# Optimization experiments

Hardware: AMD Instinct MI355X
Metric: run time of the kernel (lower is better)

## Reference

```python
import jax, jax.numpy as jnp
import numpy as np

KH = KW = 3
STRIDE = 1
PAD = 1
DIL = 1


def setup_inputs() -> dict:
    key = jax.random.key(0)
    k1, k2, k3, k4 = jax.random.split(key, 4)
    B, C, H, W = 16, 64, 64, 64
    Cout = 64
    K = KH * KW
    x = jax.random.normal(k1, (B, C, H, W), jnp.float32)
    offset = jax.random.normal(k2, (B, 2 * K, H, W), jnp.float32)
    mask = jax.random.uniform(k3, (B, K, H, W), jnp.float32)
    # uniform(-stdv, stdv) init with stdv = 1/sqrt(C*KH*KW) ~ 0.0417; scaled normal is close enough
    weight = jax.random.normal(k4, (Cout, C, KH, KW), jnp.float32) * 0.04
    bias = jnp.zeros((Cout,), jnp.float32)  # no_bias=True -> frozen zeros, still added
    return dict(input=x, offset=offset, mask=mask, weight=weight, bias=bias)


def _bilinear(img, py, px):
    # img: [C, H, W]; py, px: [K, Ho, Wo] float sampling coords
    # DCNv2 semantics: out-of-bounds corner contributions are zero.
    H, W = img.shape[1], img.shape[2]
    y0f = jnp.floor(py)
    x0f = jnp.floor(px)
    wy = py - y0f
    wx = px - x0f
    y0 = y0f.astype(jnp.int32)
    x0 = x0f.astype(jnp.int32)
    out = jnp.zeros((img.shape[0],) + py.shape, img.dtype)
    for dy in (0, 1):
        for dx in (0, 1):
            yi = y0 + dy
            xi = x0 + dx
            valid = ((yi >= 0) & (yi < H) & (xi >= 0) & (xi < W)).astype(img.dtype)
            v = img[:, jnp.clip(yi, 0, H - 1), jnp.clip(xi, 0, W - 1)]  # [C,K,Ho,Wo]
            w = (wy if dy else 1.0 - wy) * (wx if dx else 1.0 - wx)
            out = out + v * (w * valid)[None]
    return out  # [C, K, Ho, Wo]


def reference(input, offset, mask, weight, bias):
    B, C, H, W = input.shape
    Cout, _, kh, kw = weight.shape
    K = kh * kw
    Ho = (H + 2 * PAD - (DIL * (kh - 1) + 1)) // STRIDE + 1
    Wo = (W + 2 * PAD - (DIL * (kw - 1) + 1)) // STRIDE + 1
    off = offset.reshape(B, K, 2, Ho, Wo)  # per kernel point: (dy, dx)
    ky = jnp.repeat(jnp.arange(kh), kw)  # [K] kernel row index
    kx = jnp.tile(jnp.arange(kw), kh)    # [K] kernel col index
    base_y = jnp.arange(Ho) * STRIDE - PAD
    base_x = jnp.arange(Wo) * STRIDE - PAD
    py = off[:, :, 0] + (base_y[None, None, :, None] + (ky * DIL)[None, :, None, None])
    px = off[:, :, 1] + (base_x[None, None, None, :] + (kx * DIL)[None, :, None, None])
    sampled = jax.vmap(_bilinear)(input, py, px)        # [B, C, K, Ho, Wo]
    modulated = sampled * mask[:, None]                 # mask-modulated accumulation
    out = jnp.einsum('bckpq,ock->bopq', modulated, weight.reshape(Cout, C, K))
    return out + bias[None, :, None, None]
```

## Files before the change

### kernel.cpp

```cpp
#include <hip/hip_runtime.h>
#include <hip/hip_fp16.h>

#define BATCH 16
#define C_IN  64
#define HH    64
#define WW    64
#define COUT  64
#define KK    9
#define HW    4096
#define CK    576
#define MROW  200

typedef _Float16 f16x8 __attribute__((ext_vector_type(8)));
typedef float    f32x4 __attribute__((ext_vector_type(4)));

__device__ __forceinline__ unsigned short f32_to_f16u(float f) {
    _Float16 h = (_Float16)f;
    unsigned short u;
    __builtin_memcpy(&u, &h, 2);
    return u;
}

__device__ __forceinline__ __half2 as_h2(unsigned int u) {
    __half2 r; __builtin_memcpy(&r, &u, 4); return r;
}
__device__ __forceinline__ unsigned int as_u32(__half2 v) {
    unsigned int u; __builtin_memcpy(&u, &v, 4); return u;
}

__global__ __launch_bounds__(256) void prep_kernel(
    const float* __restrict__ x, const float* __restrict__ w,
    unsigned short* __restrict__ xt, unsigned short* __restrict__ wt) {
    __shared__ unsigned short tile[64][72];
    const int t = threadIdx.x;
    const int blk = blockIdx.x;
    if (blk < 1024) {
        const int b = blk >> 6, y = blk & 63;
        const float* xrow = x + ((b * 64) * 64 + y) * 64;
#pragma unroll
        for (int it = 0; it < 4; ++it) {
            const int idx = it * 256 + t;
            const int c = idx >> 4, seg = idx & 15;
            const float4 v = *(const float4*)(xrow + c * HW + seg * 4);
            tile[seg * 4 + 0][c] = f32_to_f16u(v.x);
            tile[seg * 4 + 1][c] = f32_to_f16u(v.y);
            tile[seg * 4 + 2][c] = f32_to_f16u(v.z);
            tile[seg * 4 + 3][c] = f32_to_f16u(v.w);
        }
        __syncthreads();
#pragma unroll
        for (int it = 0; it < 2; ++it) {
            const int idx = it * 256 + t;
            const int xx = idx >> 3, cs = idx & 7;
            *(int4*)&xt[((b * HW) + y * 64 + xx) * 64 + cs * 8] =
                *(const int4*)&tile[xx][cs * 8];
        }
    } else {
        const int i = (blk - 1024) * 256 + t;
        const int j = i & 7;
        const int l = (i >> 3) & 63;
        const int ot = (i >> 9) & 3;
        const int r = i >> 11;
        const int ks = r % 6, kc = r / 6;
        const int o  = ot * 16 + (l & 15);
        const int kk = ks * 32 + (l >> 4) * 8 + j;
        const int tap = kk >> 6, c = kk & 63;
        const int k = kc * 3 + tap;
        wt[i] = f32_to_f16u(w[o * CK + c * KK + k]);
    }
}

__global__ __launch_bounds__(128, 4) void dcn_main_kernel(
    const float* __restrict__ offset, const float* __restrict__ mask,
    const unsigned short* __restrict__ xt, const unsigned short* __restrict__ wt,
    const float* __restrict__ bias, float* __restrict__ out) {
    __shared__ __align__(16) unsigned short Mlds[2][16 * MROW];
    __shared__ __align__(16) int PWw[2][144 * 4];
    __shared__ __align__(8) unsigned short PWa[2][144 * 4];

    const int t    = threadIdx.x;
    const int wave = __builtin_amdgcn_readfirstlane(t >> 6);
    const int lane = t & 63;
    const int quad = lane >> 4, m16 = lane & 15;

    const int blk = blockIdx.x;
    const int xcd = blk & 7;
    const int i8  = blk >> 3;
    const int s   = ((i8 & 31) << 3) | (i8 >> 5);
    const int b   = (xcd << 1) | (s >> 7);
    const int rr  = s & 127;
    const int row = rr >> 1;
    const int qbase = (rr & 1) * 32 + wave * 16;

    f32x4 acc[4];
#pragma unroll
    for (int ot = 0; ot < 4; ++ot)
#pragma unroll
        for (int r = 0; r < 4; ++r) acc[ot][r] = 0.f;

    const float* offb = offset + b * (2 * KK * HW) + row * 64;
    const float* mb   = mask + b * (KK * HW) + row * 64;
    const char* xtb   = (const char*)(xt + b * (HW * 64));
    char* MW = (char*)Mlds[wave];
    const int lg  = lane >> 3;
    const int co2 = (lane & 7) * 16;

#pragma unroll
    for (int p = 0; p < 3; ++p) {
        if (lane < 48) {
            const int t3  = lane >> 4;
            const int tap = p * 3 + t3;
            const int pxi = lane & 15;
            const int q = qbase + pxi;
            const float oy = offb[(2 * tap) * HW + q];
            const float ox = offb[(2 * tap + 1) * HW + q];
            const float mk = mb[tap * HW + q];
            const float py  = oy + (float)(row - 1 + p);
            const float pxf = ox + (float)(q - 1 + t3);
            const float y0f = floorf(py), x0f = floorf(pxf);
            const float wy = py - y0f, wx = pxf - x0f;
            const int y0 = (int)y0f, x0 = (int)x0f;
            const int y1 = y0 + 1,   x1 = x0 + 1;
            const float vy0 = (y0 >= 0 && y0 < HH) ? 1.f : 0.f;
            const float vy1 = (y1 >= 0 && y1 < HH) ? 1.f : 0.f;
            const float vx0 = (x0 >= 0 && x0 < WW) ? 1.f : 0.f;
            const float vx1 = (x1 >= 0 && x1 < WW) ? 1.f : 0.f;
            const float w00 = (1.f - wy) * (1.f - wx) * vy0 * vx0 * mk;
            const float w01 = (1.f - wy) * wx         * vy0 * vx1 * mk;
            const float w10 = wy * (1.f - wx)         * vy1 * vx0 * mk;
            const float w11 = wy * wx                 * vy1 * vx1 * mk;
            const int cy0 = min(max(y0, 0), HH - 1), cy1 = min(max(y1, 0), HH - 1);
            const int cx0 = min(max(x0, 0), WW - 1), cx1 = min(max(x1, 0), WW - 1);
            const int it = tap * 16 + pxi;
            const unsigned int s00 = f32_to_f16u(w00);
            const unsigned int s01 = f32_to_f16u(w01);
            const unsigned int s10 = f32_to_f16u(w10);
            const unsigned int s11 = f32_to_f16u(w11);
            int4 P0;
            P0.x = (int)(s00 | (s00 << 16));
            P0.y = (int)(s01 | (s01 << 16));
            P0.z = (int)(s10 | (s10 << 16));
            P0.w = (int)(s11 | (s11 << 16));
            *(int4*)&PWw[wave][it * 4] = P0;
            ushort4 A;
            A.x = (unsigned short)(cy0 * 64 + cx0);
            A.y = (unsigned short)(cy0 * 64 + cx1);
            A.z = (unsigned short)(cy1 * 64 + cx0);
            A.w = (unsigned short)(cy1 * 64 + cx1);
            *(ushort4*)&PWa[wave][it * 4] = A;
        }
    }

    uint4 g[6][4];

    auto bload = [&](int kc) {
        const unsigned short* Pa = &PWa[wave][0] + 48 * kc * 4;
#pragma unroll
        for (int i = 0; i < 6; ++i) {
            const int l = i * 8 + lg;
            const ushort4 a = *(const ushort4*)(Pa + l * 4);
            g[i][0] = *(const uint4*)(xtb + ((int)a.x << 7) + co2);
            g[i][1] = *(const uint4*)(xtb + ((int)a.y << 7) + co2);
            g[i][2] = *(const uint4*)(xtb + ((int)a.z << 7) + co2);
            g[i][3] = *(const uint4*)(xtb + ((int)a.w << 7) + co2);
        }
    };

    auto bfinish = [&](int kc) {
        const int* Pw = &PWw[wave][0] + 48 * kc * 4;
#pragma unroll
        for (int i = 0; i < 6; ++i) {
            const int l = i * 8 + lg;
            const int4 p0 = *(const int4*)(Pw + l * 4);
            const __half2 c00 = as_h2((unsigned)p0.x);
            const __half2 c01 = as_h2((unsigned)p0.y);
            const __half2 c10 = as_h2((unsigned)p0.z);
            const __half2 c11 = as_h2((unsigned)p0.w);
            const uint4 q0 = g[i][0], q1 = g[i][1], q2 = g[i][2], q3 = g[i][3];
            uint4 ov;
            {
                __half2 v = __hmul2(c00, as_h2(q0.x));
                v = __hfma2(c01, as_h2(q1.x), v);
                v = __hfma2(c10, as_h2(q2.x), v);
                v = __hfma2(c11, as_h2(q3.x), v);
                ov.x = as_u32(v);
            }
            {
                __half2 v = __hmul2(c00, as_h2(q0.y));
                v = __hfma2(c01, as_h2(q1.y), v);
                v = __hfma2(c10, as_h2(q2.y), v);
                v = __hfma2(c11, as_h2(q3.y), v);
                ov.y = as_u32(v);
            }
            {
                __half2 v = __hmul2(c00, as_h2(q0.z));
                v = __hfma2(c01, as_h2(q1.z), v);
                v = __hfma2(c10, as_h2(q2.z), v);
                v = __hfma2(c11, as_h2(q3.z), v);
                ov.z = as_u32(v);
            }
            {
                __half2 v = __hmul2(c00, as_h2(q0.w));
                v = __hfma2(c01, as_h2(q1.w), v);
                v = __hfma2(c10, as_h2(q2.w), v);
                v = __hfma2(c11, as_h2(q3.w), v);
                ov.w = as_u32(v);
            }
            *(uint4*)(MW + (l & 15) * 400 + (l >> 4) * 128 + co2) = ov;
        }
    };

    auto phaseC = [&](int kc) {
        const unsigned short* wkc = wt + kc * (6 * 4 * 512);
#pragma unroll
        for (int ks = 0; ks < 6; ++ks) {
            const f16x8 bfrag =
                *(const f16x8*)(MW + m16 * 400 + ks * 64 + quad * 16);
#pragma unroll
            for (int ot = 0; ot < 4; ++ot) {
                const f16x8 afrag =
                    *(const f16x8*)(wkc + (ks * 4 + ot) * 512 + lane * 8);
                acc[ot] = __builtin_amdgcn_mfma_f32_16x16x32_f16(afrag, bfrag,
                                                                 acc[ot], 0, 0, 0);
            }
        }
    };

    bload(0);
    __builtin_amdgcn_sched_barrier(0);
    for (int kc = 0; kc < 3; ++kc) {
        bfinish(kc);
        if (kc < 2) {
            bload(kc + 1);
            __builtin_amdgcn_sched_barrier(0);
        }
        phaseC(kc);
    }

    float* ob = out + b * (COUT * HW) + row * 64 + qbase + m16;
#pragma unroll
    for (int ot = 0; ot < 4; ++ot)
#pragma unroll
        for (int r = 0; r < 4; ++r) {
            const int o = ot * 16 + quad * 4 + r;
            ob[o * HW] = acc[ot][r] + bias[o];
        }
}

extern "C" void kernel_launch(void* const* d_in, const int* in_sizes, int n_in,
                              void* d_out, int out_size, void* d_ws,
                              size_t ws_size, hipStream_t stream) {
    const float* x    = (const float*)d_in[0];
    const float* off  = (const float*)d_in[1];
    const float* mask = (const float*)d_in[2];
    const float* w    = (const float*)d_in[3];
    const float* bias = (const float*)d_in[4];
    float* out = (float*)d_out;

    unsigned short* xt = (unsigned short*)d_ws;
    unsigned short* wt = (unsigned short*)((char*)d_ws + 8388608);

    prep_kernel<<<1024 + 144, 256, 0, stream>>>(x, w, xt, wt);
    dcn_main_kernel<<<2048, 128, 0, stream>>>(off, mask, xt, wt, bias, out);
}
```

Baseline: 108.2 us.

## Stage 13-row input window in LDS via async loads, gather from shared memory

Each block now covers a full output row with four waves and copies a 13-row window of the transposed fp16 input into LDS using global_load_lds. Bilinear corner gathers then read from LDS, and only samples whose rows fall outside the window go back to global memory. The goal is to replace scattered global gathers with LDS reads and reuse the rows shared by the pixels in a row. In exchange it uses about 128KB of LDS (one block per CU), drops the software prefetch pipeline, adds a barrier, and pays the up-front window load.

Measured after the change: 108.7 us. About the same (+0.5%).

```diff
diff --git a/kernel.cpp b/kernel.cpp
--- a/kernel.cpp
+++ b/kernel.cpp
@@ -10,6 +10,8 @@
 #define HW    4096
 #define CK    576
 #define MROW  200
+#define WROWS 13
+#define WLO   6
 
 typedef _Float16 f16x8 __attribute__((ext_vector_type(8)));
 typedef float    f32x4 __attribute__((ext_vector_type(4)));
@@ -70,13 +72,15 @@
     }
 }
 
-__global__ __launch_bounds__(128, 4) void dcn_main_kernel(
+__global__ __launch_bounds__(256, 1) void dcn_main_kernel(
     const float* __restrict__ offset, const float* __restrict__ mask,
     const unsigned short* __restrict__ xt, const unsigned short* __restrict__ wt,
     const float* __restrict__ bias, float* __restrict__ out) {
-    __shared__ __align__(16) unsigned short Mlds[2][16 * MROW];
-    __shared__ __align__(16) int PWw[2][144 * 4];
-    __shared__ __align__(8) unsigned short PWa[2][144 * 4];
+    __shared__ __align__(16) unsigned short win[WROWS * 64 * 64];
+    __shared__ __align__(16) unsigned short Mlds[4][16 * MROW];
+    __shared__ __align__(16) int PWw[576 * 4];
+    __shared__ __align__(8) unsigned short PWa[576 * 4];
+    __shared__ __align__(8) unsigned short PWg[576 * 4];
 
     const int t    = threadIdx.x;
     const int wave = __builtin_amdgcn_readfirstlane(t >> 6);
@@ -85,38 +89,52 @@
 
     const int blk = blockIdx.x;
     const int xcd = blk & 7;
-    const int i8  = blk >> 3;
-    const int s   = ((i8 & 31) << 3) | (i8 >> 5);
-    const int b   = (xcd << 1) | (s >> 7);
-    const int rr  = s & 127;
-    const int row = rr >> 1;
-    const int qbase = (rr & 1) * 32 + wave * 16;
-
-    f32x4 acc[4];
-#pragma unroll
-    for (int ot = 0; ot < 4; ++ot)
-#pragma unroll
-        for (int r = 0; r < 4; ++r) acc[ot][r] = 0.f;
+    const int i7  = blk >> 3;
+    const int b   = (xcd << 1) | (i7 >> 6);
+    const int row = i7 & 63;
+    const int qbase = wave * 16;
 
     const float* offb = offset + b * (2 * KK * HW) + row * 64;
     const float* mb   = mask + b * (KK * HW) + row * 64;
     const char* xtb   = (const char*)(xt + b * (HW * 64));
-    char* MW = (char*)Mlds[wave];
-    const int lg  = lane >> 3;
-    const int co2 = (lane & 7) * 16;
-
+
+    float oyv[3], oxv[3], mkv[3];
 #pragma unroll
     for (int p = 0; p < 3; ++p) {
-        if (lane < 48) {
-            const int t3  = lane >> 4;
-            const int tap = p * 3 + t3;
-            const int pxi = lane & 15;
-            const int q = qbase + pxi;
-            const float oy = offb[(2 * tap) * HW + q];
-            const float ox = offb[(2 * tap + 1) * HW + q];
-            const float mk = mb[tap * HW + q];
-            const float py  = oy + (float)(row - 1 + p);
-            const float pxf = ox + (float)(q - 1 + t3);
+        const int it = p * 256 + t;
+        if (it < 576) {
+            const int tap = it >> 6, q = it & 63;
+            oyv[p] = offb[(2 * tap) * HW + q];
+            oxv[p] = offb[(2 * tap + 1) * HW + q];
+            mkv[p] = mb[tap * HW + q];
+        } else { oyv[p] = 0.f; oxv[p] = 0.f; mkv[p] = 0.f; }
+    }
+    asm volatile("" :: "v"(oyv[0]), "v"(oxv[0]), "v"(mkv[0]),
+                       "v"(oyv[1]), "v"(oxv[1]), "v"(mkv[1]),
+                       "v"(oyv[2]), "v"(oxv[2]), "v"(mkv[2]));
+
+#pragma unroll
+    for (int s = 0; s < 2 * WROWS; ++s) {
+        const int slot = s >> 1;
+        const int srcrow = min(max(row - WLO + slot, 0), HH - 1);
+        const char* src = xtb + srcrow * 8192 + (s & 1) * 4096 + t * 16;
+        __builtin_amdgcn_global_load_lds(
+            (const __attribute__((address_space(1))) unsigned int*)src,
+            (__attribute__((address_space(3))) unsigned int*)
+                ((char*)win + s * 4096 + t * 16),
+            16, 0, 0);
+    }
+    __builtin_amdgcn_sched_barrier(0);
+
+#pragma unroll
+    for (int p = 0; p < 3; ++p) {
+        const int it = p * 256 + t;
+        if (it < 576) {
+            const int tap = it >> 6, q = it & 63;
+            const int ky = (tap * 11) >> 5;
+            const int kx = tap - ky * 3;
+            const float py  = oyv[p] + (float)(row - 1 + ky);
+            const float pxf = oxv[p] + (float)(q - 1 + kx);
             const float y0f = floorf(py), x0f = floorf(pxf);
             const float wy = py - y0f, wx = pxf - x0f;
             const int y0 = (int)y0f, x0 = (int)x0f;
@@ -125,13 +143,18 @@
             const float vy1 = (y1 >= 0 && y1 < HH) ? 1.f : 0.f;
             const float vx0 = (x0 >= 0 && x0 < WW) ? 1.f : 0.f;
             const float vx1 = (x1 >= 0 && x1 < WW) ? 1.f : 0.f;
+            const float mk = mkv[p];
             const float w00 = (1.f - wy) * (1.f - wx) * vy0 * vx0 * mk;
             const float w01 = (1.f - wy) * wx         * vy0 * vx1 * mk;
             const float w10 = wy * (1.f - wx)         * vy1 * vx0 * mk;
             const float w11 = wy * wx                 * vy1 * vx1 * mk;
             const int cy0 = min(max(y0, 0), HH - 1), cy1 = min(max(y1, 0), HH - 1);
             const int cx0 = min(max(x0, 0), WW - 1), cx1 = min(max(x1, 0), WW - 1);
-            const int it = tap * 16 + pxi;
+            const int sl0 = cy0 - (row - WLO);
+            const int sl1 = cy1 - (row - WLO);
+            const int esc = (sl0 < 0) | (sl1 > (WROWS - 1));
+            const int c0 = min(max(sl0, 0), WROWS - 1);
+            const int c1 = min(max(sl1, 0), WROWS - 1);
             const unsigned int s00 = f32_to_f16u(w00);
             const unsigned int s01 = f32_to_f16u(w01);
             const unsigned int s10 = f32_to_f16u(w10);
@@ -141,42 +164,59 @@
             P0.y = (int)(s01 | (s01 << 16));
             P0.z = (int)(s10 | (s10 << 16));
             P0.w = (int)(s11 | (s11 << 16));
-            *(int4*)&PWw[wave][it * 4] = P0;
+            *(int4*)&PWw[it * 4] = P0;
             ushort4 A;
-            A.x = (unsigned short)(cy0 * 64 + cx0);
-            A.y = (unsigned short)(cy0 * 64 + cx1);
-            A.z = (unsigned short)(cy1 * 64 + cx0);
-            A.w = (unsigned short)(cy1 * 64 + cx1);
-            *(ushort4*)&PWa[wave][it * 4] = A;
-        }
-    }
-
-    uint4 g[6][4];
-
-    auto bload = [&](int kc) {
-        const unsigned short* Pa = &PWa[wave][0] + 48 * kc * 4;
+            A.x = (unsigned short)((c0 * 64 + cx0) | (esc << 15));
+            A.y = (unsigned short)(c0 * 64 + cx1);
+            A.z = (unsigned short)(c1 * 64 + cx0);
+            A.w = (unsigned short)(c1 * 64 + cx1);
+            *(ushort4*)&PWa[it * 4] = A;
+            ushort4 G;
+            G.x = (unsigned short)(cy0 * 64 + cx0);
+            G.y = (unsigned short)(cy0 * 64 + cx1);
+            G.z = (unsigned short)(cy1 * 64 + cx0);
+            G.w = (unsigned short)(cy1 * 64 + cx1);
+            *(ushort4*)&PWg[it * 4] = G;
+        }
+    }
+    __syncthreads();
+
+    f32x4 acc[4];
+#pragma unroll
+    for (int ot = 0; ot < 4; ++ot)
+#pragma unroll
+        for (int r = 0; r < 4; ++r) acc[ot][r] = 0.f;
+
+    char* MW = (char*)Mlds[wave];
+    const int lg  = lane >> 3;
+    const int co2 = (lane & 7) * 16;
+
+#pragma unroll
+    for (int kc = 0; kc < 3; ++kc) {
 #pragma unroll
         for (int i = 0; i < 6; ++i) {
-            const int l = i * 8 + lg;
-            const ushort4 a = *(const ushort4*)(Pa + l * 4);
-            g[i][0] = *(const uint4*)(xtb + ((int)a.x << 7) + co2);
-            g[i][1] = *(const uint4*)(xtb + ((int)a.y << 7) + co2);
-            g[i][2] = *(const uint4*)(xtb + ((int)a.z << 7) + co2);
-            g[i][3] = *(const uint4*)(xtb + ((int)a.w << 7) + co2);
-        }
-    };
-
-    auto bfinish = [&](int kc) {
-        const int* Pw = &PWw[wave][0] + 48 * kc * 4;
-#pragma unroll
-        for (int i = 0; i < 6; ++i) {
-            const int l = i * 8 + lg;
-            const int4 p0 = *(const int4*)(Pw + l * 4);
+            const int l  = i * 8 + lg;
+            const int it = (3 * kc + (l >> 4)) * 64 + qbase + (l & 15);
+            const ushort4 a = *(const ushort4*)&PWa[it * 4];
+            const int4 p0   = *(const int4*)&PWw[it * 4];
+            uint4 q0 = *(const uint4*)((const char*)win + (((int)a.x & 0x7FFF) << 7) + co2);
+            uint4 q1 = *(const uint4*)((const char*)win + (((int)a.y) << 7) + co2);
+            uint4 q2 = *(const uint4*)((const char*)win + (((int)a.z) << 7) + co2);
+            uint4 q3 = *(const uint4*)((const char*)win + (((int)a.w) << 7) + co2);
+            const bool esc = (a.x & 0x8000u) != 0;
+            if (__builtin_expect(__any(esc), 0)) {
+                if (esc) {
+                    const ushort4 ga = *(const ushort4*)&PWg[it * 4];
+                    q0 = *(const uint4*)(xtb + ((int)ga.x << 7) + co2);
+                    q1 = *(const uint4*)(xtb + ((int)ga.y << 7) + co2);
+                    q2 = *(const uint4*)(xtb + ((int)ga.z << 7) + co2);
+                    q3 = *(const uint4*)(xtb + ((int)ga.w << 7) + co2);
+                }
+            }
             const __half2 c00 = as_h2((unsigned)p0.x);
             const __half2 c01 = as_h2((unsigned)p0.y);
             const __half2 c10 = as_h2((unsigned)p0.z);
             const __half2 c11 = as_h2((unsigned)p0.w);
-            const uint4 q0 = g[i][0], q1 = g[i][1], q2 = g[i][2], q3 = g[i][3];
             uint4 ov;
             {
                 __half2 v = __hmul2(c00, as_h2(q0.x));
@@ -208,9 +248,6 @@
             }
             *(uint4*)(MW + (l & 15) * 400 + (l >> 4) * 128 + co2) = ov;
         }
-    };
-
-    auto phaseC = [&](int kc) {
         const unsigned short* wkc = wt + kc * (6 * 4 * 512);
 #pragma unroll
         for (int ks = 0; ks < 6; ++ks) {
@@ -224,17 +261,6 @@
                                                                  acc[ot], 0, 0, 0);
             }
         }
-    };
-
-    bload(0);
-    __builtin_amdgcn_sched_barrier(0);
-    for (int kc = 0; kc < 3; ++kc) {
-        bfinish(kc);
-        if (kc < 2) {
-            bload(kc + 1);
-            __builtin_amdgcn_sched_barrier(0);
-        }
-        phaseC(kc);
     }
 
     float* ob = out + b * (COUT * HW) + row * 64 + qbase + m16;
@@ -261,5 +287,5 @@
     unsigned short* wt = (unsigned short*)((char*)d_ws + 8388608);
 
     prep_kernel<<<1024 + 144, 256, 0, stream>>>(x, w, xt, wt);
-    dcn_main_kernel<<<2048, 128, 0, stream>>>(off, mask, xt, wt, bias, out);
-}
+    dcn_main_kernel<<<1024, 256, 0, stream>>>(off, mask, xt, wt, bias, out);
+}
```
